# Performance work log

Measured on AMD Instinct MI355X. Metric: run time of the kernel, lower is better.

Reference implementation:

```python
import jax, jax.numpy as jnp
import numpy as np

N_NODES = 50000
N_EDGES = 800000
D = 128

def setup_inputs() -> dict:
    key = jax.random.key(0)
    k1, k2, k3, k4 = jax.random.split(key, 4)
    x = jax.random.normal(k1, (N_NODES, D), dtype=jnp.float32)
    edge_index = jax.random.randint(k2, (2, N_EDGES), 0, N_NODES, dtype=jnp.int64)
    # nn.Linear params: W is (out_dim, in_dim), b is (out_dim,)
    W = jax.random.normal(k3, (D, D), dtype=jnp.float32) * (1.0 / np.sqrt(D))
    b = jax.random.normal(k4, (D,), dtype=jnp.float32) * 0.01
    return {"x": x, "edge_index": edge_index, "W": W, "b": b}

def reference(x, edge_index, W, b):
    row, col = edge_index[0], edge_index[1]
    h = x @ W.T + b                      # (N, D) linear projection
    msgs = h[col]                        # gather by source col, (E, D)
    agg = jax.ops.segment_sum(msgs, row, num_segments=N_NODES)  # scatter-add by row
    return agg + h                       # residual
```

## Files before the change

### kernel.cpp

```cpp
#include <hip/hip_runtime.h>

#define NN 50000
#define NE 800000
#define DD 128

#define NBUCK 782
#define CAPB 1280
#define NBA 64
#define NBC 192
#define TPB_PREP 1024
#define EITER 13
#define ASTRIDE 132

typedef __attribute__((ext_vector_type(8))) short short8;
typedef __attribute__((ext_vector_type(4))) float f32x4;

__device__ __forceinline__ unsigned short f2bf(float f) {
    unsigned int u = __float_as_uint(f);
    u += 0x7fffu + ((u >> 16) & 1u);
    return (unsigned short)(u >> 16);
}

#define ACCUM8(a, pq)                                   \
    a[0] += __uint_as_float((pq).x << 16);              \
    a[1] += __uint_as_float((pq).x & 0xffff0000u);      \
    a[2] += __uint_as_float((pq).y << 16);              \
    a[3] += __uint_as_float((pq).y & 0xffff0000u);      \
    a[4] += __uint_as_float((pq).z << 16);              \
    a[5] += __uint_as_float((pq).z & 0xffff0000u);      \
    a[6] += __uint_as_float((pq).w << 16);              \
    a[7] += __uint_as_float((pq).w & 0xffff0000u);

__global__ __launch_bounds__(1024) void prep(
    const float* __restrict__ x, unsigned short* __restrict__ xbf,
    const float* __restrict__ W, unsigned short* __restrict__ Wbf,
    const int* __restrict__ ei, unsigned int* __restrict__ binned,
    int* __restrict__ cursor)
{
    __shared__ int cnt[NBUCK];
    __shared__ int off[NBUCK];
    const int t = threadIdx.x;

    if (blockIdx.x < NBA) {
        if (t < NBUCK) cnt[t] = 0;
        __syncthreads();

        int rr[EITER], cc[EITER];
#pragma unroll
        for (int q = 0; q < EITER; ++q) {
            const int e = blockIdx.x * TPB_PREP + t + q * (NBA * TPB_PREP);
            rr[q] = (e < NE) ? ei[e] : -1;
            cc[q] = (e < NE) ? ei[NE + e] : 0;
        }
#pragma unroll
        for (int q = 0; q < EITER; ++q)
            if (rr[q] >= 0) atomicAdd(&cnt[rr[q] >> 6], 1);
        __syncthreads();

        if (t < NBUCK) off[t] = atomicAdd(&cursor[t], cnt[t]);
        __syncthreads();

#pragma unroll
        for (int q = 0; q < EITER; ++q) {
            if (rr[q] >= 0) {
                const int bk = rr[q] >> 6;
                const int p = atomicAdd(&off[bk], 1);
                if (p < CAPB)
                    binned[(size_t)bk * CAPB + p] =
                        ((unsigned)(rr[q] & 63) << 16) | (unsigned)cc[q];
            }
        }
        return;
    }

    const int ct = (blockIdx.x - NBA) * TPB_PREP + t;
    for (int i = ct; i < NN * DD / 4; i += NBC * TPB_PREP) {
        const float4 v = ((const float4*)x)[i];
        ushort4 s;
        s.x = f2bf(v.x); s.y = f2bf(v.y); s.z = f2bf(v.z); s.w = f2bf(v.w);
        ((ushort4*)xbf)[i] = s;
    }
    if (blockIdx.x == NBA) {
        for (int i = t; i < DD * DD / 4; i += TPB_PREP) {
            const float4 v = ((const float4*)W)[i];
            ushort4 s;
            s.x = f2bf(v.x); s.y = f2bf(v.y); s.z = f2bf(v.z); s.w = f2bf(v.w);
            ((ushort4*)Wbf)[i] = s;
        }
    }
}

__global__ __launch_bounds__(512) void aggemm(
    const unsigned short* __restrict__ xbf,
    const unsigned short* __restrict__ Wbf, const float* __restrict__ bias,
    const int* __restrict__ cursor, const unsigned int* __restrict__ binned,
    float* __restrict__ out)
{
    __shared__ float acc_l[64 * ASTRIDE];
    __shared__ unsigned int elist[CAPB];
    __shared__ int cnt_l[64];
    __shared__ int start_l[64];
    __shared__ int off_l[64];

    const int b     = blockIdx.x;
    const int node0 = b << 6;
    const int t     = threadIdx.x;
    const int wave  = t >> 6;
    const int lane  = t & 63;

    if (t < 64) cnt_l[t] = 0;
    __syncthreads();

    int cntb = cursor[b];
    if (cntb > CAPB) cntb = CAPB;
    const unsigned int* bptr = binned + (size_t)b * CAPB;

    unsigned int ue[3];
#pragma unroll
    for (int q = 0; q < 3; ++q) {
        const int e = q * 512 + t;
        ue[q] = 0u;
        if (e < cntb) {
            ue[q] = bptr[e];
            atomicAdd(&cnt_l[(ue[q] >> 16) & 63], 1);
        }
    }
    __syncthreads();

    if (t < 64) {
        const int orig = cnt_l[t];
        int v = orig;
#pragma unroll
        for (int d = 1; d < 64; d <<= 1) {
            const int o = __shfl_up(v, d, 64);
            if (t >= d) v += o;
        }
        start_l[t] = v - orig;
        off_l[t]   = v - orig;
    }
    __syncthreads();

#pragma unroll
    for (int q = 0; q < 3; ++q) {
        const int e = q * 512 + t;
        if (e < cntb) {
            const int p = atomicAdd(&off_l[(ue[q] >> 16) & 63], 1);
            elist[p] = ue[q];
        }
    }
    __syncthreads();

    const int g = lane >> 4;
    const int s = lane & 15;

#pragma unroll
    for (int r2 = 0; r2 < 8; ++r2) {
        const int ln = wave * 8 + r2;
        const int st = start_l[ln];
        const int dn = cnt_l[ln];
        const int grow = node0 + ln;

        uint4 sv = (uint4){0u, 0u, 0u, 0u};
        if (g == 0 && grow < NN)
            sv = *(const uint4*)(xbf + (size_t)grow * 128 + s * 8);

        float a[8];
#pragma unroll
        for (int i = 0; i < 8; ++i) a[i] = 0.f;

        const int nq = (dn + 3) >> 2;

        uint4 p[8];
#pragma unroll
        for (int q = 0; q < 8; ++q) {
            const int e = q * 4 + g;
            p[q] = (uint4){0u, 0u, 0u, 0u};
            if (q < nq && e < dn) {
                const unsigned u = elist[st + e];
                p[q] = *(const uint4*)(xbf + (size_t)(u & 0xffffu) * 128 + s * 8);
            }
        }
#pragma unroll
        for (int q = 0; q < 8; ++q)
            if (q < nq) { ACCUM8(a, p[q]); }

        for (int k = 32; k < dn; k += 16) {
            uint4 pp[4];
#pragma unroll
            for (int q = 0; q < 4; ++q) {
                const int e = k + q * 4 + g;
                pp[q] = (uint4){0u, 0u, 0u, 0u};
                if (e < dn) {
                    const unsigned u = elist[st + e];
                    pp[q] = *(const uint4*)(xbf + (size_t)(u & 0xffffu) * 128 + s * 8);
                }
            }
#pragma unroll
            for (int q = 0; q < 4; ++q) { ACCUM8(a, pp[q]); }
        }

#pragma unroll
        for (int i = 0; i < 8; ++i) a[i] += __shfl_xor(a[i], 16, 64);
#pragma unroll
        for (int i = 0; i < 8; ++i) a[i] += __shfl_xor(a[i], 32, 64);

        if (g == 0) {
            ACCUM8(a, sv);
            *(float4*)&acc_l[ln * ASTRIDE + s * 8]     = (float4){a[0], a[1], a[2], a[3]};
            *(float4*)&acc_l[ln * ASTRIDE + s * 8 + 4] = (float4){a[4], a[5], a[6], a[7]};
            if (s == 0) acc_l[ln * ASTRIDE + 128] = (float)(dn + 1);
        }
    }
    __syncthreads();

    const int m16  = lane & 15;
    const int quad = lane >> 4;
    const int rowt = (wave & 3) * 16;
    const int colb = (wave >> 2) * 64;

    short8 af[4];
#pragma unroll
    for (int kc = 0; kc < 4; ++kc) {
        const float* src = &acc_l[(rowt + m16) * ASTRIDE + kc * 32 + quad * 8];
        const float4 a0 = *(const float4*)src;
        const float4 a1 = *(const float4*)(src + 4);
        short8 a;
        a[0] = (short)f2bf(a0.x); a[1] = (short)f2bf(a0.y);
        a[2] = (short)f2bf(a0.z); a[3] = (short)f2bf(a0.w);
        a[4] = (short)f2bf(a1.x); a[5] = (short)f2bf(a1.y);
        a[6] = (short)f2bf(a1.z); a[7] = (short)f2bf(a1.w);
        af[kc] = a;
    }

    f32x4 ac[4];
#pragma unroll
    for (int nt = 0; nt < 4; ++nt) ac[nt] = (f32x4){0.f, 0.f, 0.f, 0.f};

#pragma unroll
    for (int kc = 0; kc < 4; ++kc) {
#pragma unroll
        for (int nt = 0; nt < 4; ++nt) {
            const short8 bf = *(const short8*)(
                Wbf + (size_t)(colb + nt * 16 + m16) * 128 + kc * 32 + quad * 8);
            ac[nt] = __builtin_amdgcn_mfma_f32_16x16x32_bf16(af[kc], bf, ac[nt], 0, 0, 0);
        }
    }

    float bv[4];
#pragma unroll
    for (int nt = 0; nt < 4; ++nt) bv[nt] = bias[colb + nt * 16 + m16];

#pragma unroll
    for (int r = 0; r < 4; ++r) {
        const int lr   = rowt + quad * 4 + r;
        const int grow = node0 + lr;
        if (grow < NN) {
            const float cd = acc_l[lr * ASTRIDE + 128];
#pragma unroll
            for (int nt = 0; nt < 4; ++nt)
                out[(size_t)grow * 128 + colb + nt * 16 + m16] = ac[nt][r] + cd * bv[nt];
        }
    }
}

extern "C" void kernel_launch(void* const* d_in, const int* in_sizes, int n_in,
                              void* d_out, int out_size, void* d_ws, size_t ws_size,
                              hipStream_t stream)
{
    const float* x  = (const float*)d_in[0];
    const int*   ei = (const int*)d_in[1];
    const float* W  = (const float*)d_in[2];
    const float* b  = (const float*)d_in[3];
    float* out = (float*)d_out;

    unsigned short* xbf    = (unsigned short*)d_ws;
    unsigned int*   binned = (unsigned int*)(xbf + (size_t)NN * DD);
    unsigned short* Wbf    = (unsigned short*)(binned + (size_t)NBUCK * CAPB);
    int*            cursor = (int*)(Wbf + DD * DD);

    hipMemsetAsync(cursor, 0, NBUCK * sizeof(int), stream);

    prep<<<NBA + NBC, TPB_PREP, 0, stream>>>(x, xbf, W, Wbf, ei, binned, cursor);

    aggemm<<<NBUCK, 512, 0, stream>>>(xbf, Wbf, b, cursor, binned, out);
}
```

Before: 140.2 us.

## Replace global atomic bucket cursors with per-block fixed slices and bf16 LDS staging

The binning stage no longer claims bucket offsets through global atomics on a memset cursor array. Each of 128 binning blocks now writes into its own 32-entry slice per bucket and records a byte count per (block, bucket). The aggregation kernel reads the 128 counts and loads the 4096 slots with vector loads, masking out unused ones. This removes the memset launch and global atomic contention. The aggregated rows are also stored in LDS as bf16 rather than fp32, which cuts shared memory and lets launch_bounds request more occupancy. The risks are silent dropping of edges when a block sees more than 32 edges for one bucket, and more slot data read per bucket.

```diff
diff --git a/kernel.cpp b/kernel.cpp
--- a/kernel.cpp
+++ b/kernel.cpp
@@ -5,12 +5,14 @@
 #define DD 128
 
 #define NBUCK 782
-#define CAPB 1280
-#define NBA 64
+#define NBA 128
 #define NBC 192
 #define TPB_PREP 1024
-#define EITER 13
-#define ASTRIDE 132
+#define EITER 7
+#define SLICE 32
+#define BINSTRIDE (NBA * SLICE)
+#define ELCAP 1536
+#define ABSTRIDE 136
 
 typedef __attribute__((ext_vector_type(8))) short short8;
 typedef __attribute__((ext_vector_type(4))) float f32x4;
@@ -35,14 +37,14 @@
     const float* __restrict__ x, unsigned short* __restrict__ xbf,
     const float* __restrict__ W, unsigned short* __restrict__ Wbf,
     const int* __restrict__ ei, unsigned int* __restrict__ binned,
-    int* __restrict__ cursor)
+    unsigned char* __restrict__ cntarr)
 {
     __shared__ int cnt[NBUCK];
     __shared__ int off[NBUCK];
     const int t = threadIdx.x;
 
     if (blockIdx.x < NBA) {
-        if (t < NBUCK) cnt[t] = 0;
+        if (t < NBUCK) { cnt[t] = 0; off[t] = 0; }
         __syncthreads();
 
         int rr[EITER], cc[EITER];
@@ -57,19 +59,20 @@
             if (rr[q] >= 0) atomicAdd(&cnt[rr[q] >> 6], 1);
         __syncthreads();
 
-        if (t < NBUCK) off[t] = atomicAdd(&cursor[t], cnt[t]);
-        __syncthreads();
-
 #pragma unroll
         for (int q = 0; q < EITER; ++q) {
             if (rr[q] >= 0) {
                 const int bk = rr[q] >> 6;
                 const int p = atomicAdd(&off[bk], 1);
-                if (p < CAPB)
-                    binned[(size_t)bk * CAPB + p] =
+                if (p < SLICE)
+                    binned[(size_t)bk * BINSTRIDE + blockIdx.x * SLICE + p] =
                         ((unsigned)(rr[q] & 63) << 16) | (unsigned)cc[q];
             }
         }
+        __syncthreads();
+        for (int i = t; i < NBUCK; i += TPB_PREP)
+            cntarr[(size_t)blockIdx.x * NBUCK + i] =
+                (unsigned char)min(cnt[i], SLICE);
         return;
     }
 
@@ -90,17 +93,19 @@
     }
 }
 
-__global__ __launch_bounds__(512) void aggemm(
+__global__ __launch_bounds__(512, 8) void aggemm(
     const unsigned short* __restrict__ xbf,
     const unsigned short* __restrict__ Wbf, const float* __restrict__ bias,
-    const int* __restrict__ cursor, const unsigned int* __restrict__ binned,
-    float* __restrict__ out)
+    const unsigned char* __restrict__ cntarr,
+    const unsigned int* __restrict__ binned, float* __restrict__ out)
 {
-    __shared__ float acc_l[64 * ASTRIDE];
-    __shared__ unsigned int elist[CAPB];
+    __shared__ unsigned short accb[64 * ABSTRIDE];
+    __shared__ unsigned int elist[ELCAP];
+    __shared__ int scnt[NBA];
     __shared__ int cnt_l[64];
     __shared__ int start_l[64];
     __shared__ int off_l[64];
+    __shared__ int degl[64];
 
     const int b     = blockIdx.x;
     const int node0 = b << 6;
@@ -108,22 +113,20 @@
     const int wave  = t >> 6;
     const int lane  = t & 63;
 
+    if (t < NBA) scnt[t] = cntarr[(size_t)t * NBUCK + b];
     if (t < 64) cnt_l[t] = 0;
     __syncthreads();
 
-    int cntb = cursor[b];
-    if (cntb > CAPB) cntb = CAPB;
-    const unsigned int* bptr = binned + (size_t)b * CAPB;
-
-    unsigned int ue[3];
-#pragma unroll
-    for (int q = 0; q < 3; ++q) {
-        const int e = q * 512 + t;
-        ue[q] = 0u;
-        if (e < cntb) {
-            ue[q] = bptr[e];
-            atomicAdd(&cnt_l[(ue[q] >> 16) & 63], 1);
-        }
+    const unsigned int* bptr = binned + (size_t)b * BINSTRIDE;
+    const uint4 u0 = *(const uint4*)(bptr + t * 8);
+    const uint4 u1 = *(const uint4*)(bptr + t * 8 + 4);
+    unsigned ue[8] = {u0.x, u0.y, u0.z, u0.w, u1.x, u1.y, u1.z, u1.w};
+    bool val[8];
+#pragma unroll
+    for (int j = 0; j < 8; ++j) {
+        const int slot = t * 8 + j;
+        val[j] = (slot & (SLICE - 1)) < scnt[slot / SLICE];
+        if (val[j]) atomicAdd(&cnt_l[(ue[j] >> 16) & 63], 1);
     }
     __syncthreads();
 
@@ -141,11 +144,10 @@
     __syncthreads();
 
 #pragma unroll
-    for (int q = 0; q < 3; ++q) {
-        const int e = q * 512 + t;
-        if (e < cntb) {
-            const int p = atomicAdd(&off_l[(ue[q] >> 16) & 63], 1);
-            elist[p] = ue[q];
+    for (int j = 0; j < 8; ++j) {
+        if (val[j]) {
+            const int p = atomicAdd(&off_l[(ue[j] >> 16) & 63], 1);
+            if (p < ELCAP) elist[p] = ue[j];
         }
     }
     __syncthreads();
@@ -206,9 +208,11 @@
 
         if (g == 0) {
             ACCUM8(a, sv);
-            *(float4*)&acc_l[ln * ASTRIDE + s * 8]     = (float4){a[0], a[1], a[2], a[3]};
-            *(float4*)&acc_l[ln * ASTRIDE + s * 8 + 4] = (float4){a[4], a[5], a[6], a[7]};
-            if (s == 0) acc_l[ln * ASTRIDE + 128] = (float)(dn + 1);
+            short8 w;
+#pragma unroll
+            for (int i = 0; i < 8; ++i) w[i] = (short)f2bf(a[i]);
+            *(short8*)&accb[ln * ABSTRIDE + s * 8] = w;
+            if (s == 0) degl[ln] = dn + 1;
         }
     }
     __syncthreads();
@@ -220,17 +224,8 @@
 
     short8 af[4];
 #pragma unroll
-    for (int kc = 0; kc < 4; ++kc) {
-        const float* src = &acc_l[(rowt + m16) * ASTRIDE + kc * 32 + quad * 8];
-        const float4 a0 = *(const float4*)src;
-        const float4 a1 = *(const float4*)(src + 4);
-        short8 a;
-        a[0] = (short)f2bf(a0.x); a[1] = (short)f2bf(a0.y);
-        a[2] = (short)f2bf(a0.z); a[3] = (short)f2bf(a0.w);
-        a[4] = (short)f2bf(a1.x); a[5] = (short)f2bf(a1.y);
-        a[6] = (short)f2bf(a1.z); a[7] = (short)f2bf(a1.w);
-        af[kc] = a;
-    }
+    for (int kc = 0; kc < 4; ++kc)
+        af[kc] = *(const short8*)&accb[(rowt + m16) * ABSTRIDE + kc * 32 + quad * 8];
 
     f32x4 ac[4];
 #pragma unroll
@@ -255,7 +250,7 @@
         const int lr   = rowt + quad * 4 + r;
         const int grow = node0 + lr;
         if (grow < NN) {
-            const float cd = acc_l[lr * ASTRIDE + 128];
+            const float cd = (float)degl[lr];
 #pragma unroll
             for (int nt = 0; nt < 4; ++nt)
                 out[(size_t)grow * 128 + colb + nt * 16 + m16] = ac[nt][r] + cd * bv[nt];
@@ -275,12 +270,10 @@
 
     unsigned short* xbf    = (unsigned short*)d_ws;
     unsigned int*   binned = (unsigned int*)(xbf + (size_t)NN * DD);
-    unsigned short* Wbf    = (unsigned short*)(binned + (size_t)NBUCK * CAPB);
-    int*            cursor = (int*)(Wbf + DD * DD);
-
-    hipMemsetAsync(cursor, 0, NBUCK * sizeof(int), stream);
-
-    prep<<<NBA + NBC, TPB_PREP, 0, stream>>>(x, xbf, W, Wbf, ei, binned, cursor);
-
-    aggemm<<<NBUCK, 512, 0, stream>>>(xbf, Wbf, b, cursor, binned, out);
-}
+    unsigned short* Wbf    = (unsigned short*)(binned + (size_t)NBUCK * BINSTRIDE);
+    unsigned char*  cntarr = (unsigned char*)(Wbf + DD * DD);
+
+    prep<<<NBA + NBC, TPB_PREP, 0, stream>>>(x, xbf, W, Wbf, ei, binned, cntarr);
+
+    aggemm<<<NBUCK, 512, 0, stream>>>(xbf, Wbf, b, cntarr, binned, out);
+}
```

After: 137.9 us. No clear change (-1.7%).
